# Kernel optimization log

Hardware: AMD Instinct MI355X
Metric: run time of the kernel (lower is better)

## Reference

```python
import jax, jax.numpy as jnp
import numpy as np

N_NODES = 100000


def gcn_conv(x, W, b, src, dst, n):
    # PyG GCNConv: linear transform, add self-loops, symmetric deg^-1/2 norm,
    # scatter-sum messages from src -> dst, add bias.
    x = x @ W  # [N, out]
    loop = jnp.arange(n, dtype=src.dtype)
    src_sl = jnp.concatenate([src, loop])
    dst_sl = jnp.concatenate([dst, loop])
    deg = jax.ops.segment_sum(jnp.ones_like(dst_sl, dtype=x.dtype), dst_sl, num_segments=n)
    dinv = jax.lax.rsqrt(deg)
    norm = dinv[src_sl] * dinv[dst_sl]  # [E+N]
    msg = x[src_sl] * norm[:, None]
    out = jax.ops.segment_sum(msg, dst_sl, num_segments=n)
    return out + b


def base_gnn(x, edge_index, W1, b1, W2, b2):
    src, dst = edge_index[0], edge_index[1]
    n = x.shape[0]
    h = gcn_conv(x, W1, b1, src, dst, n)
    h = jax.nn.relu(h)
    return gcn_conv(h, W2, b2, src, dst, n)


def setup_inputs() -> dict:
    key = jax.random.key(0)
    ks = jax.random.split(key, 12)
    n, e, ep, en = N_NODES, 1600000, 200000, 200000
    in_ch, hid, out_ch, n_classes = 256, 128, 128, 10
    x = jax.random.normal(ks[0], (n, in_ch), dtype=jnp.float32)
    edge_index = jax.random.randint(ks[1], (2, e), 0, n, dtype=jnp.int64)
    edge_index_pos = jax.random.randint(ks[2], (2, ep), 0, n, dtype=jnp.int64)
    edge_index_neg = jax.random.randint(ks[3], (2, en), 0, n, dtype=jnp.int64)
    s1 = 1.0 / np.sqrt(in_ch)
    s2 = 1.0 / np.sqrt(hid)
    so = 1.0 / np.sqrt(out_ch)
    sl = 1.0 / np.sqrt(2 * out_ch)
    return {
        "x": x,
        "edge_index": edge_index,
        "edge_index_pos": edge_index_pos,
        "edge_index_neg": edge_index_neg,
        "W1": jax.random.uniform(ks[4], (in_ch, hid), jnp.float32, -s1, s1),
        "b1": jnp.zeros((hid,), jnp.float32),
        "W2": jax.random.uniform(ks[5], (hid, out_ch), jnp.float32, -s2, s2),
        "b2": jnp.zeros((out_ch,), jnp.float32),
        "Wcls": jax.random.uniform(ks[6], (out_ch, n_classes), jnp.float32, -so, so),
        "bcls": jax.random.uniform(ks[7], (n_classes,), jnp.float32, -so, so),
        "Wlink": jax.random.uniform(ks[8], (2 * out_ch, 1), jnp.float32, -sl, sl),
        "blink": jax.random.uniform(ks[9], (1,), jnp.float32, -sl, sl),
    }


def reference(x, edge_index, edge_index_pos, edge_index_neg,
              W1, b1, W2, b2, Wcls, bcls, Wlink, blink):
    # Shared base embedding (math identical to torch's redundant recompute)
    h = base_gnn(x, edge_index, W1, b1, W2, b2)  # [N, 128]
    # Node head
    node_logits = jax.nn.relu(h) @ Wcls + bcls
    node_pred = jax.nn.log_softmax(node_logits, axis=1)
    # Link head: gather endpoint embeddings, concat, linear
    xp = jnp.concatenate([h[edge_index_pos[0]], h[edge_index_pos[1]]], axis=1)
    xn = jnp.concatenate([h[edge_index_neg[0]], h[edge_index_neg[1]]], axis=1)
    link_pos = (xp @ Wlink + blink)[:, 0]
    link_neg = (xn @ Wlink + blink)[:, 0]
    return (node_pred, link_pos, link_neg)
```

## Files before the change

kernel.cpp:

```cpp
#include <hip/hip_runtime.h>
#include <stdint.h>

typedef __attribute__((ext_vector_type(8))) short bf16x8;
typedef __attribute__((ext_vector_type(4))) float f32x4;

__device__ __forceinline__ float b2f(uint32_t h) {
    union { uint32_t u; float f; } v; v.u = h << 16; return v.f;
}
__device__ __forceinline__ ushort f2b(float f) {
    union { float f; uint32_t u; } v; v.f = f;
    uint32_t u = v.u;
    return (ushort)((u + 0x7fffu + ((u >> 16) & 1u)) >> 16);
}
__device__ __forceinline__ float ldin(const void* p, int i, int fp32) {
    return fp32 ? ((const float*)p)[i] : b2f(((const ushort*)p)[i]);
}

__device__ __forceinline__ void sniff(const void* W1, const void* ei, int* sf) {
    if (threadIdx.x < 64) {
        int l = threadIdx.x;
        const ushort* w = (const ushort*)W1;
        bool bad = !(fabsf(b2f(w[l])) <= 0.25f) || !(fabsf(b2f(w[64 + l])) <= 0.25f);
        unsigned long long mb = __ballot(bad);
        const int* e = (const int*)ei;
        bool z = (l < 16) ? (e[2 * l + 1] == 0) : false;
        unsigned long long mz = __ballot(z);
        if (l == 0) {
            sf[0] = mb ? 1 : 0;
            sf[1] = (__popcll(mz & 0xffffull) >= 15) ? 1 : 0;
        }
    }
    __syncthreads();
}


__global__ __launch_bounds__(256) void k_prep(const void* __restrict__ x,
                                              const void* ei, const void* ep, const void* en,
                                              const void* W1, const void* b1, const void* W2,
                                              const void* b2, const void* Wc, const void* bc,
                                              const void* Wl, const void* bl,
                                              int* cEi, int* cEp, int* cEn,
                                              ushort* __restrict__ xc,
                                              ushort* Wt1, ushort* Wt2, ushort* WtC,
                                              ushort* b1c, ushort* b2c, ushort* bcc,
                                              ushort* Wlc, ushort* blc,
                                              int twoE, int twoEp, int twoEn, int N,
                                              int Bidx, int Bw) {
    __shared__ int sf[2];
    sniff(W1, ei, sf);
    int f = sf[0], i64 = sf[1];
    int b = blockIdx.x;

    if (b < Bidx) {
        int i = (b * 256 + threadIdx.x) * 2;
        const void* srcp; int* dstp; int j = i;
        if (i < twoE) { srcp = ei; dstp = cEi; }
        else if (i < twoE + twoEp) { srcp = ep; dstp = cEp; j = i - twoE; }
        else if (i < twoE + twoEp + twoEn) { srcp = en; dstp = cEn; j = i - twoE - twoEp; }
        else return;
        int v0, v1;
        if (i64) {
            longlong2 t = *(const longlong2*)((const long long*)srcp + j);
            v0 = (int)t.x; v1 = (int)t.y;
        } else {
            int2 t = *(const int2*)((const int*)srcp + j);
            v0 = t.x; v1 = t.y;
        }
        v0 = v0 < 0 ? 0 : (v0 >= N ? N - 1 : v0);
        v1 = v1 < 0 ? 0 : (v1 >= N ? N - 1 : v1);
        *(int2*)(dstp + j) = make_int2(v0, v1);
    } else if (b < Bidx + Bw) {
        int i = (b - Bidx) * 256 + threadIdx.x;
        if (i < 32768) {
            int c = i >> 8, kpos = i & 255;
            int s = kpos >> 5, t = kpos & 31, q = t >> 3, jj = t & 7;
            int k = s * 32 + (jj < 4 ? q * 4 + jj : 16 + q * 4 + (jj - 4));
            Wt1[i] = f2b(ldin(W1, k * 128 + c, f));
        } else if (i < 49152) {
            int j = i - 32768, c = j >> 7, k = j & 127;
            Wt2[j] = f2b(ldin(W2, k * 128 + c, f));
        } else if (i < 51200) {
            int j = i - 49152, c = j >> 7, k = j & 127;
            ushort v = 0;
            if (c < 10) v = f2b(ldin(Wc, k * 10 + c, f));
            WtC[j] = v;
        } else if (i < 51328) {
            int j = i - 51200; b1c[j] = f2b(ldin(b1, j, f));
        } else if (i < 51456) {
            int j = i - 51328; b2c[j] = f2b(ldin(b2, j, f));
        } else if (i < 51472) {
            int j = i - 51456;
            ushort v = 0;
            if (j < 10) v = f2b(ldin(bc, j, f));
            bcc[j] = v;
        } else if (i < 51728) {
            int j = i - 51472; Wlc[j] = f2b(ldin(Wl, j, f));
        } else if (i < 51736) {
            int j = i - 51728;
            ushort v = 0;
            if (j < 1) v = f2b(ldin(bl, 0, f));
            blc[j] = v;
        }
    } else {
        int gw = (b - Bidx - Bw) * 4 + (threadIdx.x >> 6);
        int ntile = (N + 15) >> 4;
        if (gw >= ntile * 4) return;
        int tile = gw >> 2, s2 = gw & 3;
        int l = threadIdx.x & 63, mr = l & 15, q = l >> 4;
        int row = tile * 16 + mr;
        if (row > N - 1) row = N - 1;
#pragma unroll
        for (int u = 0; u < 2; ++u) {
            int s = s2 * 2 + u;
            uint4 o;
            if (f) {
                const float* xf = (const float*)x + (size_t)row * 256 + s * 32;
                float4 a = *(const float4*)(xf + q * 4);
                float4 bb = *(const float4*)(xf + 16 + q * 4);
                o.x = (uint32_t)f2b(a.x) | ((uint32_t)f2b(a.y) << 16);
                o.y = (uint32_t)f2b(a.z) | ((uint32_t)f2b(a.w) << 16);
                o.z = (uint32_t)f2b(bb.x) | ((uint32_t)f2b(bb.y) << 16);
                o.w = (uint32_t)f2b(bb.z) | ((uint32_t)f2b(bb.w) << 16);
            } else {
                const ushort* xs = (const ushort*)x + (size_t)row * 256 + s * 32;
                uint2 lo = *(const uint2*)(xs + q * 4);
                uint2 hi = *(const uint2*)(xs + 16 + q * 4);
                o.x = lo.x; o.y = lo.y; o.z = hi.x; o.w = hi.y;
            }
            *(uint4*)(xc + ((size_t)(tile * 8 + s) * 64 + l) * 8) = o;
        }
    }
}

__global__ __launch_bounds__(256) void k_hist1(const int* __restrict__ dst, int* __restrict__ histM,
                                               int E, int NB1) {
    __shared__ int h[512];
    for (int j = threadIdx.x; j < 512; j += 256) h[j] = 0;
    __syncthreads();
    int base = blockIdx.x * 4096;
    for (int j = threadIdx.x; j < 4096; j += 256) {
        int i = base + j;
        if (i < E) atomicAdd(&h[dst[i] >> 8], 1);
    }
    __syncthreads();
    for (int j = threadIdx.x; j < 512; j += 256)
        histM[j * NB1 + blockIdx.x] = h[j];
}

__global__ __launch_bounds__(1024) void k_mscan_block(const int* __restrict__ in, int* __restrict__ out,
                                                      int* __restrict__ bsum, int len) {
    __shared__ int sh[1024];
    int t = threadIdx.x;
    int i = blockIdx.x * 1024 + t;
    int val = (i < len) ? in[i] : 0;
    sh[t] = val; __syncthreads();
    for (int off = 1; off < 1024; off <<= 1) {
        int v = (t >= off) ? sh[t - off] : 0;
        __syncthreads();
        sh[t] += v;
        __syncthreads();
    }
    if (i < len) out[i] = sh[t] - val;
    if (t == 1023) bsum[blockIdx.x] = sh[1023];
}

__global__ __launch_bounds__(1024) void k_mscan_topadd(int* __restrict__ out, const int* __restrict__ bsum,
                                                       int* __restrict__ cbs, int len, int mb,
                                                       int NB1, int E) {
    __shared__ int sh[1024];
    int t = threadIdx.x;
    sh[t] = (t < mb) ? bsum[t] : 0; __syncthreads();
    for (int off = 1; off < 1024; off <<= 1) {
        int v = (t >= off) ? sh[t - off] : 0;
        __syncthreads();
        sh[t] += v;
        __syncthreads();
    }
    int pref = (blockIdx.x > 0) ? sh[blockIdx.x - 1] : 0;
    int i = blockIdx.x * 1024 + t;
    if (i < len) {
        int v = out[i] + pref;
        out[i] = v;
        if (i % NB1 == 0) cbs[i / NB1] = v;
    }
    if (i == 0) cbs[512] = E;
}

__global__ __launch_bounds__(256) void k_scatter1(const int* __restrict__ src, const int* __restrict__ dst,
                                                  const int* __restrict__ off, int2* __restrict__ grouped,
                                                  int E, int NB1) {
    __shared__ int o[512];
    for (int j = threadIdx.x; j < 512; j += 256) o[j] = off[j * NB1 + blockIdx.x];
    __syncthreads();
    int base = blockIdx.x * 4096;
    for (int j = threadIdx.x; j < 4096; j += 256) {
        int i = base + j;
        if (i < E) {
            int d = dst[i];
            int p = atomicAdd(&o[d >> 8], 1);
            grouped[p] = make_int2(src[i], d);
        }
    }
}

__global__ __launch_bounds__(256) void k_deg2(const int2* __restrict__ grouped, const int* __restrict__ cbs,
                                              int* __restrict__ deg, int N) {
    __shared__ int c[256];
    c[threadIdx.x] = 0;
    __syncthreads();
    int b = blockIdx.x;
    int s0 = cbs[b], s1 = cbs[b + 1];
    for (int i = s0 + threadIdx.x; i < s1; i += 256)
        atomicAdd(&c[grouped[i].y & 255], 1);
    __syncthreads();
    int v = b * 256 + threadIdx.x;
    if (v < N) deg[v] = c[threadIdx.x];
}

__global__ __launch_bounds__(1024) void k_scan_block(const int* __restrict__ deg, int* __restrict__ rowptr,
                                                     float* __restrict__ dinv, int* __restrict__ bsum, int n) {
    __shared__ int sh[1024];
    int t = threadIdx.x;
    int i = blockIdx.x * 1024 + t;
    int val = (i < n) ? deg[i] : 0;
    sh[t] = val; __syncthreads();
    for (int off = 1; off < 1024; off <<= 1) {
        int v = (t >= off) ? sh[t - off] : 0;
        __syncthreads();
        sh[t] += v;
        __syncthreads();
    }
    if (i < n) {
        rowptr[i] = sh[t] - val;
        dinv[i] = rsqrtf((float)(val + 1));
    }
    if (t == 1023) bsum[blockIdx.x] = sh[1023];
}

__global__ __launch_bounds__(1024) void k_scan_topadd(int* __restrict__ rowptr, const int* __restrict__ bsum,
                                                      int nb, int n, int E) {
    __shared__ int sh[1024];
    int t = threadIdx.x;
    sh[t] = (t < nb) ? bsum[t] : 0; __syncthreads();
    for (int off = 1; off < 1024; off <<= 1) {
        int v = (t >= off) ? sh[t - off] : 0;
        __syncthreads();
        sh[t] += v;
        __syncthreads();
    }
    int pref = (blockIdx.x > 0) ? sh[blockIdx.x - 1] : 0;
    int i = blockIdx.x * 1024 + t;
    if (i < n) rowptr[i] += pref;
    if (i == 0) rowptr[n] = E;
}

__global__ __launch_bounds__(256) void k_fill2(const int2* __restrict__ grouped, const int* __restrict__ cbs,
                                               const int* __restrict__ rowptr, const float* __restrict__ dinv,
                                               int2* __restrict__ edge, int N) {
    __shared__ int o[256];
    int b = blockIdx.x;
    int v = b * 256 + threadIdx.x;
    o[threadIdx.x] = (v < N) ? rowptr[v] : 0;
    __syncthreads();
    int s0 = cbs[b], s1 = cbs[b + 1];
    for (int i = s0 + threadIdx.x; i < s1; i += 256) {
        int2 e = grouped[i];
        int p = atomicAdd(&o[e.y & 255], 1);
        float w = dinv[e.x] * dinv[e.y];
        edge[p] = make_int2(e.x, __float_as_int(w));
    }
}

template <int NS>
__global__ __launch_bounds__(256, 2) void k_gemm(const ushort* __restrict__ Xf,
                                                 const ushort* __restrict__ Wt,
                                                 ushort* __restrict__ Out, int nrows) {
    __shared__ uint4 sB[NS * 8 * 64];

    const int tid = threadIdx.x;
    for (int it = tid; it < NS * 8 * 64; it += 256) {
        int l = it & 63, fn = it >> 6;
        int s = fn >> 3, n = fn & 7;
        int mr = l & 15, q = l >> 4;
        sB[it] = *(const uint4*)(Wt + (size_t)(n * 16 + mr) * (NS * 32) + s * 32 + q * 8);
    }
    __syncthreads();

    const int wave = tid >> 6;
    const int l = tid & 63;
    const int q = l >> 4, mr = l & 15;
    const int gw = blockIdx.x * 4 + wave;
    const int nw = gridDim.x * 4;
    const int ntile = (nrows + 15) >> 4;

    for (int tp = gw; tp * 2 < ntile; tp += nw) {
        const int t0 = tp * 2;
        const bool has1 = (t0 + 1 < ntile);
        const int t1 = has1 ? t0 + 1 : t0;

        bf16x8 a0[NS], a1[NS];
        const ushort* x0 = Xf + ((size_t)t0 * NS * 64 + l) * 8;
        const ushort* x1 = Xf + ((size_t)t1 * NS * 64 + l) * 8;
#pragma unroll
        for (int s = 0; s < NS; ++s) a0[s] = *(const bf16x8*)(x0 + s * 512);
#pragma unroll
        for (int s = 0; s < NS; ++s) a1[s] = *(const bf16x8*)(x1 + s * 512);

        f32x4 acc0[8], acc1[8];
#pragma unroll
        for (int n = 0; n < 8; ++n) {
            acc0[n] = (f32x4){0.f, 0.f, 0.f, 0.f};
            acc1[n] = (f32x4){0.f, 0.f, 0.f, 0.f};
        }
#pragma unroll
        for (int s = 0; s < NS; ++s) {
#pragma unroll
            for (int n = 0; n < 8; ++n) {
                bf16x8 b = __builtin_bit_cast(bf16x8, sB[(s * 8 + n) * 64 + l]);
                acc0[n] = __builtin_amdgcn_mfma_f32_16x16x32_bf16(b, a0[s], acc0[n], 0, 0, 0);
                acc1[n] = __builtin_amdgcn_mfma_f32_16x16x32_bf16(b, a1[s], acc1[n], 0, 0, 0);
            }
        }
        int row0 = t0 * 16 + mr;
        if (row0 < nrows) {
            ushort* orow = Out + (size_t)row0 * 128 + q * 4;
#pragma unroll
            for (int n = 0; n < 8; ++n) {
                uint2 o;
                o.x = (uint32_t)f2b(acc0[n][0]) | ((uint32_t)f2b(acc0[n][1]) << 16);
                o.y = (uint32_t)f2b(acc0[n][2]) | ((uint32_t)f2b(acc0[n][3]) << 16);
                *(uint2*)(orow + n * 16) = o;
            }
        }
        if (has1) {
            int row1 = t1 * 16 + mr;
            if (row1 < nrows) {
                ushort* orow = Out + (size_t)row1 * 128 + q * 4;
#pragma unroll
                for (int n = 0; n < 8; ++n) {
                    uint2 o;
                    o.x = (uint32_t)f2b(acc1[n][0]) | ((uint32_t)f2b(acc1[n][1]) << 16);
                    o.y = (uint32_t)f2b(acc1[n][2]) | ((uint32_t)f2b(acc1[n][3]) << 16);
                    *(uint2*)(orow + n * 16) = o;
                }
            }
        }
    }
}

__device__ __forceinline__ void fma8(float* acc, uint4 p, float w) {
    uint32_t pu[4] = {p.x, p.y, p.z, p.w};
#pragma unroll
    for (int k = 0; k < 4; ++k) {
        float lo = __uint_as_float(pu[k] << 16);
        float hi = __uint_as_float(pu[k] & 0xffff0000u);
        acc[2 * k]     += lo * w;
        acc[2 * k + 1] += hi * w;
    }
}

__global__ __launch_bounds__(256) void k_conv(const ushort* __restrict__ XW, const int* __restrict__ rowptr,
                                              const int2* __restrict__ edge, const float* __restrict__ dinv,
                                              const ushort* __restrict__ bias, ushort* __restrict__ Hout,
                                              int n, int relu, int frag) {
    int wave = threadIdx.x >> 6;
    int v = blockIdx.x * 4 + wave;
    if (v >= n) return;
    int l = threadIdx.x & 63;
    int g = l >> 4;
    int c = l & 15;

    int s0 = rowptr[v], s1 = rowptr[v + 1];
    float dv = dinv[v];
    float wself = (g == 0) ? dv * dv : 0.f;

    uint4 pv = *(const uint4*)(XW + (size_t)v * 128 + c * 8);
    float acc[8];
    {
        uint32_t pu[4] = {pv.x, pv.y, pv.z, pv.w};
#pragma unroll
        for (int k = 0; k < 4; ++k) {
            acc[2 * k]     = __uint_as_float(pu[k] << 16) * wself;
            acc[2 * k + 1] = __uint_as_float(pu[k] & 0xffff0000u) * wself;
        }
    }

    int i = s0;
    while (i + 8 <= s1) {
        int2 eA = edge[i + g];
        int2 eB = edge[i + 4 + g];
        uint4 pA = *(const uint4*)(XW + (size_t)eA.x * 128 + c * 8);
        uint4 pB = *(const uint4*)(XW + (size_t)eB.x * 128 + c * 8);
        fma8(acc, pA, __int_as_float(eA.y));
        fma8(acc, pB, __int_as_float(eB.y));
        i += 8;
    }
    if (i + 4 <= s1) {
        int2 e = edge[i + g];
        uint4 p = *(const uint4*)(XW + (size_t)e.x * 128 + c * 8);
        fma8(acc, p, __int_as_float(e.y));
        i += 4;
    }
    if (i < s1) {
        int ei = i + g;
        bool val = ei < s1;
        int2 e = edge[val ? ei : s0];
        uint4 p = *(const uint4*)(XW + (size_t)e.x * 128 + c * 8);
        fma8(acc, p, val ? __int_as_float(e.y) : 0.f);
    }

#pragma unroll
    for (int k = 0; k < 8; ++k) {
        acc[k] += __shfl_xor(acc[k], 16);
        acc[k] += __shfl_xor(acc[k], 32);
    }

    if (g == 0) {
        uint4 bb = *(const uint4*)(bias + c * 8);
        uint32_t bu[4] = {bb.x, bb.y, bb.z, bb.w};
        uint4 o;
        uint32_t* op = (uint32_t*)&o;
#pragma unroll
        for (int k = 0; k < 4; ++k) {
            float lo = acc[2 * k]     + __uint_as_float(bu[k] << 16);
            float hi = acc[2 * k + 1] + __uint_as_float(bu[k] & 0xffff0000u);
            if (relu) { lo = fmaxf(lo, 0.f); hi = fmaxf(hi, 0.f); }
            op[k] = (uint32_t)f2b(lo) | ((uint32_t)f2b(hi) << 16);
        }
        if (frag) {
            int tile = v >> 4, mr = v & 15;
            size_t chunk = ((size_t)(tile * 4 + (c >> 2)) * 64 + (c & 3) * 16 + mr);
            *(uint4*)(Hout + chunk * 8) = o;
        } else {
            *(uint4*)(Hout + (size_t)v * 128 + c * 8) = o;
        }
    }
}

__global__ __launch_bounds__(256) void k_nodehead(const ushort* __restrict__ H, const ushort* __restrict__ WtC,
                                                  const ushort* __restrict__ bcc, const ushort* __restrict__ Wlc,
                                                  float2* __restrict__ ab, void* __restrict__ out,
                                                  int n, const void* W1s, const void* eis) {
    __shared__ int sf[2];
    sniff(W1s, eis, sf);
    int fp32o = sf[0];
    int wave = threadIdx.x >> 6;
    int gw = blockIdx.x * 4 + wave;
    if (gw * 16 >= n) return;
    int l = threadIdx.x & 63;
    int q = l >> 4, mr = l & 15;
    int m0 = gw * 16;

    const ushort* hrow = H + (size_t)(m0 + mr) * 128 + q * 8;
    bf16x8 araw[4];
#pragma unroll
    for (int s = 0; s < 4; ++s) araw[s] = *(const bf16x8*)(hrow + s * 32);

    float pa = 0.f, pb = 0.f;
#pragma unroll
    for (int s = 0; s < 4; ++s) {
        bf16x8 w0 = *(const bf16x8*)(Wlc + s * 32 + q * 8);
        bf16x8 w1 = *(const bf16x8*)(Wlc + 128 + s * 32 + q * 8);
#pragma unroll
        for (int j = 0; j < 8; ++j) {
            float hv = b2f((ushort)araw[s][j]);
            pa += hv * b2f((ushort)w0[j]);
            pb += hv * b2f((ushort)w1[j]);
        }
    }
    pa += __shfl_xor(pa, 16); pa += __shfl_xor(pa, 32);
    pb += __shfl_xor(pb, 16); pb += __shfl_xor(pb, 32);
    if (q == 0 && (m0 + mr) < n) ab[m0 + mr] = make_float2(pa, pb);

    f32x4 acc = (f32x4){0.f, 0.f, 0.f, 0.f};
#pragma unroll
    for (int s = 0; s < 4; ++s) {
        bf16x8 a = araw[s];
#pragma unroll
        for (int j = 0; j < 8; ++j) {
            ushort t = (ushort)a[j];
            if (t & 0x8000u) a[j] = 0;
        }
        bf16x8 b = *(const bf16x8*)(WtC + (size_t)mr * 128 + s * 32 + q * 8);
        acc = __builtin_amdgcn_mfma_f32_16x16x32_bf16(a, b, acc, 0, 0, 0);
    }

    float bc = b2f(bcc[mr]);
#pragma unroll
    for (int r = 0; r < 4; ++r) {
        float logit = acc[r] + bc;
        float m = (mr < 10) ? logit : -1e30f;
#pragma unroll
        for (int off = 1; off < 16; off <<= 1) m = fmaxf(m, __shfl_xor(m, off, 16));
        float ex = (mr < 10) ? expf(logit - m) : 0.f;
        float ssum = ex;
#pragma unroll
        for (int off = 1; off < 16; off <<= 1) ssum += __shfl_xor(ssum, off, 16);
        int row = m0 + q * 4 + r;
        if (mr < 10 && row < n) {
            float lsm = logit - m - logf(ssum);
            size_t idx = (size_t)row * 10 + mr;
            if (fp32o) ((float*)out)[idx] = lsm;
            else ((ushort*)out)[idx] = f2b(lsm);
        }
    }
}

__global__ __launch_bounds__(256) void k_linkfast(const float2* __restrict__ ab, const int* __restrict__ pos,
                                                  const int* __restrict__ neg, const ushort* __restrict__ blc,
                                                  void* __restrict__ out, size_t obase, int Ep, int En,
                                                  const void* W1s, const void* eis) {
    __shared__ int sf[2];
    sniff(W1s, eis, sf);
    int i = blockIdx.x * 256 + threadIdx.x;
    if (i >= Ep + En) return;
    int s, d;
    if (i < Ep) { s = pos[i]; d = pos[Ep + i]; }
    else { int j = i - Ep; s = neg[j]; d = neg[En + j]; }
    float vf = ab[s].x + ab[d].y + b2f(blc[0]);
    size_t idx = obase + (size_t)i;
    if (sf[0]) ((float*)out)[idx] = vf;
    else ((ushort*)out)[idx] = f2b(vf);
}

extern "C" void kernel_launch(void* const* d_in, const int* in_sizes, int n_in,
                              void* d_out, int out_size, void* d_ws, size_t ws_size,
                              hipStream_t stream) {
    const void* x    = d_in[0];
    const void* ei   = d_in[1];
    const void* eip  = d_in[2];
    const void* ein  = d_in[3];
    const void* W1   = d_in[4];
    const void* b1   = d_in[5];
    const void* W2   = d_in[6];
    const void* b2   = d_in[7];
    const void* Wcls = d_in[8];
    const void* bcls = d_in[9];
    const void* Wl   = d_in[10];
    const void* bl   = d_in[11];

    const int N  = in_sizes[0] / 256;
    const int E  = in_sizes[1] / 2;
    const int Ep = in_sizes[2] / 2;
    const int En = in_sizes[3] / 2;

    const int NB1  = (E + 4095) / 4096;
    const int mlen = 512 * NB1;
    const int mb   = (mlen + 1023) / 1024;
    const int ntile = (N + 15) / 16;

    char* ws = (char*)d_ws;
    size_t off = 0;
    auto alloc = [&](size_t bytes) -> void* {
        void* p = ws + off;
        off = (off + bytes + 255) & ~(size_t)255;
        return p;
    };
    ushort* xc     = (ushort*)alloc((size_t)ntile * 8 * 64 * 16);
    ushort* bufXW  = (ushort*)alloc((size_t)N * 128 * 2);
    ushort* bufH   = (ushort*)alloc((size_t)ntile * 4 * 64 * 16);
    float2* ab     = (float2*)alloc((size_t)N * 8);
    int*    cEi    = (int*)alloc((size_t)2 * E * 4);
    int*    cEp    = (int*)alloc((size_t)2 * Ep * 4);
    int*    cEn    = (int*)alloc((size_t)2 * En * 4);
    int2*   grouped= (int2*)alloc((size_t)E * 8);
    int*    histM  = (int*)alloc((size_t)mlen * 4);
    int*    offM   = (int*)alloc((size_t)mlen * 4);
    int*    msum   = (int*)alloc(4096);
    int*    cbs    = (int*)alloc(513 * 4);
    float*  dinv   = (float*)alloc((size_t)N * 4);
    int*    deg    = (int*)alloc((size_t)N * 4);
    int*    rowp   = (int*)alloc((size_t)(N + 1) * 4);
    int2*   edge   = (int2*)alloc((size_t)E * 8);
    int*    bsum   = (int*)alloc(1024);
    ushort* Wt1    = (ushort*)alloc(65536);
    ushort* Wt2    = (ushort*)alloc(32768);
    ushort* WtC    = (ushort*)alloc(4096);
    ushort* b1c    = (ushort*)alloc(256);
    ushort* b2c    = (ushort*)alloc(256);
    ushort* bcc    = (ushort*)alloc(64);
    ushort* Wlc    = (ushort*)alloc(512);
    ushort* blc    = (ushort*)alloc(64);

    int twoE = 2 * E, twoEp = 2 * Ep, twoEn = 2 * En;
    int idx_total = twoE + twoEp + twoEn;
    int Bidx = (idx_total + 511) / 512;
    int Bw   = 203;
    int Bx   = ntile;

    k_prep<<<Bidx + Bw + Bx, 256, 0, stream>>>(x, ei, eip, ein, W1, b1, W2, b2, Wcls, bcls, Wl, bl,
                                               cEi, cEp, cEn, xc, Wt1, Wt2, WtC,
                                               b1c, b2c, bcc, Wlc, blc,
                                               twoE, twoEp, twoEn, N, Bidx, Bw);

    const int* srcp = cEi;
    const int* dstp = cEi + E;

    k_hist1<<<NB1, 256, 0, stream>>>(dstp, histM, E, NB1);
    k_mscan_block<<<mb, 1024, 0, stream>>>(histM, offM, msum, mlen);
    k_mscan_topadd<<<mb, 1024, 0, stream>>>(offM, msum, cbs, mlen, mb, NB1, E);
    k_scatter1<<<NB1, 256, 0, stream>>>(srcp, dstp, offM, grouped, E, NB1);
    k_deg2<<<512, 256, 0, stream>>>(grouped, cbs, deg, N);
    int nb = (N + 1023) / 1024;
    k_scan_block<<<nb, 1024, 0, stream>>>(deg, rowp, dinv, bsum, N);
    k_scan_topadd<<<nb, 1024, 0, stream>>>(rowp, bsum, nb, N, E);
    k_fill2<<<512, 256, 0, stream>>>(grouped, cbs, rowp, dinv, edge, N);

    k_gemm<8><<<512, 256, 0, stream>>>(xc, Wt1, bufXW, N);
    k_conv<<<(N + 3) / 4, 256, 0, stream>>>(bufXW, rowp, edge, dinv, b1c, bufH, N, 1, 1);
    k_conv<<<1, 256, 0, stream>>>(bufXW, rowp, edge, dinv, b1c, bufH, 0, 1, 1);
    k_gemm<4><<<768, 256, 0, stream>>>(bufH, Wt2, bufXW, N);
    k_conv<<<(N + 3) / 4, 256, 0, stream>>>(bufXW, rowp, edge, dinv, b2c, bufH, N, 0, 0);

    int head_blocks = ((N + 15) / 16 + 3) / 4;
    k_nodehead<<<head_blocks, 256, 0, stream>>>(bufH, WtC, bcc, Wlc, ab, d_out, N, W1, ei);
    k_linkfast<<<(Ep + En + 255) / 256, 256, 0, stream>>>(ab, cEp, cEn, blc, d_out,
                                                          (size_t)N * 10, Ep, En, W1, ei);
}
```

Baseline: 483.4 us.

## Fuse histogram into prep, merge degree and scan, widen GEMM to four tiles

Moves the destination histogram into the prep kernel as extra blocks that read the raw edge index directly, so one launch and its dependency on the converted indices go away. Degree counting and the row-pointer scan are merged into a single per-bucket kernel that uses the bucket offsets, which replaces three launches. The GEMM now handles four 16-row tiles per wave to reuse each B fragment more, drops the launch-bounds occupancy hint, and sizes its grid to match. A seemingly redundant one-block conv launch is also removed. Four accumulator sets raise register pressure, which can lower occupancy.

```diff
diff --git a/kernel.cpp b/kernel.cpp
--- a/kernel.cpp
+++ b/kernel.cpp
@@ -44,9 +44,12 @@
                                               ushort* Wt1, ushort* Wt2, ushort* WtC,
                                               ushort* b1c, ushort* b2c, ushort* bcc,
                                               ushort* Wlc, ushort* blc,
+                                              int* __restrict__ histM,
                                               int twoE, int twoEp, int twoEn, int N,
-                                              int Bidx, int Bw) {
+                                              int E, int NB1,
+                                              int Bidx, int Bw, int Bx) {
     __shared__ int sf[2];
+    __shared__ int h[512];
     sniff(W1, ei, sf);
     int f = sf[0], i64 = sf[1];
     int b = blockIdx.x;
@@ -101,7 +104,7 @@
             if (j < 1) v = f2b(ldin(bl, 0, f));
             blc[j] = v;
         }
-    } else {
+    } else if (b < Bidx + Bw + Bx) {
         int gw = (b - Bidx - Bw) * 4 + (threadIdx.x >> 6);
         int ntile = (N + 15) >> 4;
         if (gw >= ntile * 4) return;
@@ -129,22 +132,23 @@
             }
             *(uint4*)(xc + ((size_t)(tile * 8 + s) * 64 + l) * 8) = o;
         }
-    }
-}
-
-__global__ __launch_bounds__(256) void k_hist1(const int* __restrict__ dst, int* __restrict__ histM,
-                                               int E, int NB1) {
-    __shared__ int h[512];
-    for (int j = threadIdx.x; j < 512; j += 256) h[j] = 0;
-    __syncthreads();
-    int base = blockIdx.x * 4096;
-    for (int j = threadIdx.x; j < 4096; j += 256) {
-        int i = base + j;
-        if (i < E) atomicAdd(&h[dst[i] >> 8], 1);
-    }
-    __syncthreads();
-    for (int j = threadIdx.x; j < 512; j += 256)
-        histM[j * NB1 + blockIdx.x] = h[j];
+    } else {
+        int b2 = b - Bidx - Bw - Bx;
+        for (int j = threadIdx.x; j < 512; j += 256) h[j] = 0;
+        __syncthreads();
+        int base = b2 * 4096;
+        for (int j = threadIdx.x; j < 4096; j += 256) {
+            int i = base + j;
+            if (i < E) {
+                int d = i64 ? (int)((const long long*)ei)[E + i] : ((const int*)ei)[E + i];
+                d = d < 0 ? 0 : (d >= N ? N - 1 : d);
+                atomicAdd(&h[d >> 8], 1);
+            }
+        }
+        __syncthreads();
+        for (int j = threadIdx.x; j < 512; j += 256)
+            histM[j * NB1 + b2] = h[j];
+    }
 }
 
 __global__ __launch_bounds__(1024) void k_mscan_block(const int* __restrict__ in, int* __restrict__ out,
@@ -203,55 +207,32 @@
     }
 }
 
-__global__ __launch_bounds__(256) void k_deg2(const int2* __restrict__ grouped, const int* __restrict__ cbs,
-                                              int* __restrict__ deg, int N) {
-    __shared__ int c[256];
-    c[threadIdx.x] = 0;
+__global__ __launch_bounds__(256) void k_degscan(const int2* __restrict__ grouped, const int* __restrict__ cbs,
+                                                 int* __restrict__ rowptr, float* __restrict__ dinv,
+                                                 int N, int E) {
+    __shared__ int cnt[256];
+    int t = threadIdx.x, b = blockIdx.x;
+    cnt[t] = 0;
     __syncthreads();
-    int b = blockIdx.x;
     int s0 = cbs[b], s1 = cbs[b + 1];
-    for (int i = s0 + threadIdx.x; i < s1; i += 256)
-        atomicAdd(&c[grouped[i].y & 255], 1);
+    for (int i = s0 + t; i < s1; i += 256)
+        atomicAdd(&cnt[grouped[i].y & 255], 1);
     __syncthreads();
-    int v = b * 256 + threadIdx.x;
-    if (v < N) deg[v] = c[threadIdx.x];
-}
-
-__global__ __launch_bounds__(1024) void k_scan_block(const int* __restrict__ deg, int* __restrict__ rowptr,
-                                                     float* __restrict__ dinv, int* __restrict__ bsum, int n) {
-    __shared__ int sh[1024];
-    int t = threadIdx.x;
-    int i = blockIdx.x * 1024 + t;
-    int val = (i < n) ? deg[i] : 0;
-    sh[t] = val; __syncthreads();
-    for (int off = 1; off < 1024; off <<= 1) {
-        int v = (t >= off) ? sh[t - off] : 0;
-        __syncthreads();
-        sh[t] += v;
-        __syncthreads();
-    }
-    if (i < n) {
-        rowptr[i] = sh[t] - val;
-        dinv[i] = rsqrtf((float)(val + 1));
-    }
-    if (t == 1023) bsum[blockIdx.x] = sh[1023];
-}
-
-__global__ __launch_bounds__(1024) void k_scan_topadd(int* __restrict__ rowptr, const int* __restrict__ bsum,
-                                                      int nb, int n, int E) {
-    __shared__ int sh[1024];
-    int t = threadIdx.x;
-    sh[t] = (t < nb) ? bsum[t] : 0; __syncthreads();
-    for (int off = 1; off < 1024; off <<= 1) {
-        int v = (t >= off) ? sh[t - off] : 0;
-        __syncthreads();
-        sh[t] += v;
-        __syncthreads();
-    }
-    int pref = (blockIdx.x > 0) ? sh[blockIdx.x - 1] : 0;
-    int i = blockIdx.x * 1024 + t;
-    if (i < n) rowptr[i] += pref;
-    if (i == 0) rowptr[n] = E;
+    int deg = cnt[t];
+    __syncthreads();
+    for (int off = 1; off < 256; off <<= 1) {
+        int vv = (t >= off) ? cnt[t - off] : 0;
+        __syncthreads();
+        cnt[t] += vv;
+        __syncthreads();
+    }
+    int excl = cnt[t] - deg;
+    int v = b * 256 + t;
+    if (v < N) {
+        rowptr[v] = s0 + excl;
+        dinv[v] = rsqrtf((float)(deg + 1));
+    }
+    if (b == 0 && t == 0) rowptr[N] = E;
 }
 
 __global__ __launch_bounds__(256) void k_fill2(const int2* __restrict__ grouped, const int* __restrict__ cbs,
@@ -272,9 +253,9 @@
 }
 
 template <int NS>
-__global__ __launch_bounds__(256, 2) void k_gemm(const ushort* __restrict__ Xf,
-                                                 const ushort* __restrict__ Wt,
-                                                 ushort* __restrict__ Out, int nrows) {
+__global__ __launch_bounds__(256) void k_gemm(const ushort* __restrict__ Xf,
+                                              const ushort* __restrict__ Wt,
+                                              ushort* __restrict__ Out, int nrows) {
     __shared__ uint4 sB[NS * 8 * 64];
 
     const int tid = threadIdx.x;
@@ -293,54 +274,87 @@
     const int nw = gridDim.x * 4;
     const int ntile = (nrows + 15) >> 4;
 
-    for (int tp = gw; tp * 2 < ntile; tp += nw) {
-        const int t0 = tp * 2;
-        const bool has1 = (t0 + 1 < ntile);
-        const int t1 = has1 ? t0 + 1 : t0;
-
-        bf16x8 a0[NS], a1[NS];
+    for (int tp = gw; tp * 4 < ntile; tp += nw) {
+        const int t0 = tp * 4;
+        const bool h1 = (t0 + 1 < ntile), h2 = (t0 + 2 < ntile), h3 = (t0 + 3 < ntile);
+        const int tb1 = h1 ? t0 + 1 : t0, tb2 = h2 ? t0 + 2 : t0, tb3 = h3 ? t0 + 3 : t0;
+
         const ushort* x0 = Xf + ((size_t)t0 * NS * 64 + l) * 8;
-        const ushort* x1 = Xf + ((size_t)t1 * NS * 64 + l) * 8;
-#pragma unroll
-        for (int s = 0; s < NS; ++s) a0[s] = *(const bf16x8*)(x0 + s * 512);
-#pragma unroll
-        for (int s = 0; s < NS; ++s) a1[s] = *(const bf16x8*)(x1 + s * 512);
-
-        f32x4 acc0[8], acc1[8];
+        const ushort* x1 = Xf + ((size_t)tb1 * NS * 64 + l) * 8;
+        const ushort* x2 = Xf + ((size_t)tb2 * NS * 64 + l) * 8;
+        const ushort* x3 = Xf + ((size_t)tb3 * NS * 64 + l) * 8;
+
+        f32x4 accA[8], accB[8], accC[8], accD[8];
 #pragma unroll
         for (int n = 0; n < 8; ++n) {
-            acc0[n] = (f32x4){0.f, 0.f, 0.f, 0.f};
-            acc1[n] = (f32x4){0.f, 0.f, 0.f, 0.f};
+            accA[n] = (f32x4){0.f, 0.f, 0.f, 0.f};
+            accB[n] = (f32x4){0.f, 0.f, 0.f, 0.f};
+            accC[n] = (f32x4){0.f, 0.f, 0.f, 0.f};
+            accD[n] = (f32x4){0.f, 0.f, 0.f, 0.f};
         }
 #pragma unroll
         for (int s = 0; s < NS; ++s) {
+            bf16x8 a0 = *(const bf16x8*)(x0 + s * 512);
+            bf16x8 a1 = *(const bf16x8*)(x1 + s * 512);
+            bf16x8 a2 = *(const bf16x8*)(x2 + s * 512);
+            bf16x8 a3 = *(const bf16x8*)(x3 + s * 512);
 #pragma unroll
             for (int n = 0; n < 8; ++n) {
-                bf16x8 b = __builtin_bit_cast(bf16x8, sB[(s * 8 + n) * 64 + l]);
-                acc0[n] = __builtin_amdgcn_mfma_f32_16x16x32_bf16(b, a0[s], acc0[n], 0, 0, 0);
-                acc1[n] = __builtin_amdgcn_mfma_f32_16x16x32_bf16(b, a1[s], acc1[n], 0, 0, 0);
+                bf16x8 bfr = __builtin_bit_cast(bf16x8, sB[(s * 8 + n) * 64 + l]);
+                accA[n] = __builtin_amdgcn_mfma_f32_16x16x32_bf16(bfr, a0, accA[n], 0, 0, 0);
+                accB[n] = __builtin_amdgcn_mfma_f32_16x16x32_bf16(bfr, a1, accB[n], 0, 0, 0);
+                accC[n] = __builtin_amdgcn_mfma_f32_16x16x32_bf16(bfr, a2, accC[n], 0, 0, 0);
+                accD[n] = __builtin_amdgcn_mfma_f32_16x16x32_bf16(bfr, a3, accD[n], 0, 0, 0);
             }
         }
-        int row0 = t0 * 16 + mr;
-        if (row0 < nrows) {
-            ushort* orow = Out + (size_t)row0 * 128 + q * 4;
-#pragma unroll
-            for (int n = 0; n < 8; ++n) {
-                uint2 o;
-                o.x = (uint32_t)f2b(acc0[n][0]) | ((uint32_t)f2b(acc0[n][1]) << 16);
-                o.y = (uint32_t)f2b(acc0[n][2]) | ((uint32_t)f2b(acc0[n][3]) << 16);
-                *(uint2*)(orow + n * 16) = o;
-            }
-        }
-        if (has1) {
-            int row1 = t1 * 16 + mr;
-            if (row1 < nrows) {
-                ushort* orow = Out + (size_t)row1 * 128 + q * 4;
+        {
+            int row = t0 * 16 + mr;
+            if (row < nrows) {
+                ushort* orow = Out + (size_t)row * 128 + q * 4;
 #pragma unroll
                 for (int n = 0; n < 8; ++n) {
                     uint2 o;
-                    o.x = (uint32_t)f2b(acc1[n][0]) | ((uint32_t)f2b(acc1[n][1]) << 16);
-                    o.y = (uint32_t)f2b(acc1[n][2]) | ((uint32_t)f2b(acc1[n][3]) << 16);
+                    o.x = (uint32_t)f2b(accA[n][0]) | ((uint32_t)f2b(accA[n][1]) << 16);
+                    o.y = (uint32_t)f2b(accA[n][2]) | ((uint32_t)f2b(accA[n][3]) << 16);
+                    *(uint2*)(orow + n * 16) = o;
+                }
+            }
+        }
+        if (h1) {
+            int row = tb1 * 16 + mr;
+            if (row < nrows) {
+                ushort* orow = Out + (size_t)row * 128 + q * 4;
+#pragma unroll
+                for (int n = 0; n < 8; ++n) {
+                    uint2 o;
+                    o.x = (uint32_t)f2b(accB[n][0]) | ((uint32_t)f2b(accB[n][1]) << 16);
+                    o.y = (uint32_t)f2b(accB[n][2]) | ((uint32_t)f2b(accB[n][3]) << 16);
+                    *(uint2*)(orow + n * 16) = o;
+                }
+            }
+        }
+        if (h2) {
+            int row = tb2 * 16 + mr;
+            if (row < nrows) {
+                ushort* orow = Out + (size_t)row * 128 + q * 4;
+#pragma unroll
+                for (int n = 0; n < 8; ++n) {
+                    uint2 o;
+                    o.x = (uint32_t)f2b(accC[n][0]) | ((uint32_t)f2b(accC[n][1]) << 16);
+                    o.y = (uint32_t)f2b(accC[n][2]) | ((uint32_t)f2b(accC[n][3]) << 16);
+                    *(uint2*)(orow + n * 16) = o;
+                }
+            }
+        }
+        if (h3) {
+            int row = tb3 * 16 + mr;
+            if (row < nrows) {
+                ushort* orow = Out + (size_t)row * 128 + q * 4;
+#pragma unroll
+                for (int n = 0; n < 8; ++n) {
+                    uint2 o;
+                    o.x = (uint32_t)f2b(accD[n][0]) | ((uint32_t)f2b(accD[n][1]) << 16);
+                    o.y = (uint32_t)f2b(accD[n][2]) | ((uint32_t)f2b(accD[n][3]) << 16);
                     *(uint2*)(orow + n * 16) = o;
                 }
             }
@@ -569,10 +583,8 @@
     int*    msum   = (int*)alloc(4096);
     int*    cbs    = (int*)alloc(513 * 4);
     float*  dinv   = (float*)alloc((size_t)N * 4);
-    int*    deg    = (int*)alloc((size_t)N * 4);
     int*    rowp   = (int*)alloc((size_t)(N + 1) * 4);
     int2*   edge   = (int2*)alloc((size_t)E * 8);
-    int*    bsum   = (int*)alloc(1024);
     ushort* Wt1    = (ushort*)alloc(65536);
     ushort* Wt2    = (ushort*)alloc(32768);
     ushort* WtC    = (ushort*)alloc(4096);
@@ -588,28 +600,26 @@
     int Bw   = 203;
     int Bx   = ntile;
 
-    k_prep<<<Bidx + Bw + Bx, 256, 0, stream>>>(x, ei, eip, ein, W1, b1, W2, b2, Wcls, bcls, Wl, bl,
-                                               cEi, cEp, cEn, xc, Wt1, Wt2, WtC,
-                                               b1c, b2c, bcc, Wlc, blc,
-                                               twoE, twoEp, twoEn, N, Bidx, Bw);
+    k_prep<<<Bidx + Bw + Bx + NB1, 256, 0, stream>>>(x, ei, eip, ein, W1, b1, W2, b2, Wcls, bcls, Wl, bl,
+                                                     cEi, cEp, cEn, xc, Wt1, Wt2, WtC,
+                                                     b1c, b2c, bcc, Wlc, blc, histM,
+                                                     twoE, twoEp, twoEn, N, E, NB1,
+                                                     Bidx, Bw, Bx);
 
     const int* srcp = cEi;
     const int* dstp = cEi + E;
 
-    k_hist1<<<NB1, 256, 0, stream>>>(dstp, histM, E, NB1);
     k_mscan_block<<<mb, 1024, 0, stream>>>(histM, offM, msum, mlen);
     k_mscan_topadd<<<mb, 1024, 0, stream>>>(offM, msum, cbs, mlen, mb, NB1, E);
     k_scatter1<<<NB1, 256, 0, stream>>>(srcp, dstp, offM, grouped, E, NB1);
-    k_deg2<<<512, 256, 0, stream>>>(grouped, cbs, deg, N);
-    int nb = (N + 1023) / 1024;
-    k_scan_block<<<nb, 1024, 0, stream>>>(deg, rowp, dinv, bsum, N);
-    k_scan_topadd<<<nb, 1024, 0, stream>>>(rowp, bsum, nb, N, E);
+    k_degscan<<<512, 256, 0, stream>>>(grouped, cbs, rowp, dinv, N, E);
     k_fill2<<<512, 256, 0, stream>>>(grouped, cbs, rowp, dinv, edge, N);
 
-    k_gemm<8><<<512, 256, 0, stream>>>(xc, Wt1, bufXW, N);
+    int quads = (ntile + 3) / 4;
+    int g1 = (quads + 3) / 4; if (g1 > 768) g1 = 768;
+    k_gemm<8><<<g1, 256, 0, stream>>>(xc, Wt1, bufXW, N);
     k_conv<<<(N + 3) / 4, 256, 0, stream>>>(bufXW, rowp, edge, dinv, b1c, bufH, N, 1, 1);
-    k_conv<<<1, 256, 0, stream>>>(bufXW, rowp, edge, dinv, b1c, bufH, 0, 1, 1);
-    k_gemm<4><<<768, 256, 0, stream>>>(bufH, Wt2, bufXW, N);
+    k_gemm<4><<<g1, 256, 0, stream>>>(bufH, Wt2, bufXW, N);
     k_conv<<<(N + 3) / 4, 256, 0, stream>>>(bufXW, rowp, edge, dinv, b2c, bufH, N, 0, 0);
 
     int head_blocks = ((N + 15) / 16 + 3) / 4;
```

Result: faster. 453.8 us (-6.1%).
